# Performance work log

Hardware: AMD Instinct MI355X
Metric: run time of the kernel (lower is better)

The kernel has to match this reference:

```python
import jax, jax.numpy as jnp
from jax import lax
import numpy as np
import math

# --- static equivariant-conv basis (kernel lattice offsets) ---
K = 5          # kernel size = diameter / step
NRB = 3        # num_radial_basis
RMAX = 2.5     # diameter / 2
C0, C1 = 32, 16   # hidden irreps: 32x0e + 16x1e (4*ne scalars + 2*ne vectors, ne=8)
GATES = C1        # one 0e gate scalar per gated vector irrep

_c = np.arange(K, dtype=np.float32) - K // 2
_grid = np.stack(np.meshgrid(_c, _c, _c, indexing='ij'), -1)            # [K,K,K,3]
_norm = np.linalg.norm(_grid, axis=-1)
_mask = (_norm <= RMAX).astype(np.float32)
_ctr = np.linspace(0.0, RMAX, NRB).astype(np.float32)
_w = RMAX / (NRB - 1)
R_BASIS = jnp.asarray(np.exp(-(((_norm[..., None] - _ctr) / _w) ** 2)) * _mask[..., None])  # [K,K,K,NRB]
_safe = np.where(_norm == 0.0, 1.0, _norm)
_y1 = (math.sqrt(3.0) * _grid / _safe[..., None]).astype(np.float32)    # component-normalized l=1 SH
_y1[_norm == 0.0] = 0.0
Y1_SH = jnp.asarray(_y1)                                                # [K,K,K,3]
_levi = np.zeros((3, 3, 3), np.float32)
for _a, _b, _d in ((0, 1, 2), (1, 2, 0), (2, 0, 1)):
    _levi[_a, _b, _d] = 1.0
    _levi[_a, _d, _b] = -1.0
LEVI = jnp.asarray(_levi)


def _equiv_conv(x, ss, sv, vs, vv0, vv1):
    """Equivariant voxel conv: kernel = radial(|r|) * Y_l(r) * CG, then 3D conv.
    x: [B,D,H,W, C0 + 3*C1] -> [B,D,H,W, Cso + 3*Cvo]."""
    Cso, Cvo = ss.shape[-1], sv.shape[-1]
    Kss = jnp.einsum('xyzr,rio->xyzio', R_BASIS, ss)                      # 0e->0e via Y0
    Ksv = jnp.einsum('xyzr,rio,xyzm->xyziom', R_BASIS, sv, Y1_SH)         # 0e->1  via Y1
    Kvs = jnp.einsum('xyzr,rio,xyzm->xyzimo', R_BASIS, vs, Y1_SH) / math.sqrt(3.0)  # 1->0 (dot CG)
    Kvv0 = jnp.einsum('xyzr,rio->xyzio', R_BASIS, vv0)                    # 1->1 via Y0 (identity CG)
    Kvv1 = jnp.einsum('xyzr,rio->xyzio', R_BASIS, vv1)                    # 1->1 via Y1 (cross CG)
    E1 = jnp.einsum('xyzm,amb->xyzab', Y1_SH, LEVI) / math.sqrt(2.0)
    eye = jnp.eye(3, dtype=x.dtype)
    Kvv = (Kvv0[..., :, None, :, None] * eye[None, None, None, None, :, None, :]
           + Kvv1[..., :, None, :, None] * E1[..., None, :, None, :])     # [K,K,K,C1,3,Cvo,3]
    top = jnp.concatenate([Kss, Ksv.reshape(K, K, K, C0, 3 * Cvo)], axis=-1)
    bot = jnp.concatenate([Kvs.reshape(K, K, K, 3 * C1, Cso),
                           Kvv.reshape(K, K, K, 3 * C1, 3 * Cvo)], axis=-1)
    kern = jnp.concatenate([top, bot], axis=-2)                            # [K,K,K,Fin,Fout]
    return lax.conv_general_dilated(x, kern, (1, 1, 1), 'SAME',
                                    dimension_numbers=('NDHWC', 'DHWIO', 'NDHWC'))


def _gate(y):
    """e3nn Gate: activation on scalars, sigmoid(gates) scales the vectors."""
    s = jax.nn.relu(y[..., :C0])
    g = jax.nn.sigmoid(y[..., C0:C0 + GATES])
    v = y[..., C0 + GATES:].reshape(y.shape[:-1] + (C1, 3)) * g[..., None]
    return jnp.concatenate([s, v.reshape(y.shape[:-1] + (3 * C1,))], axis=-1)


def _up2(a, axes=(1, 2, 3)):
    for ax in axes:
        a = jnp.repeat(a, 2, axis=ax)
    return a


def _forward(x, c1_ss, c1_sv, c1_vs, c1_vv0, c1_vv1,
             c2_ss, c2_sv, c2_vs, c2_vv0, c2_vv1, w_pos, wl_s, wl_v):
    # --- ConvolutionBlock: two equivariant convs, each followed by a Gate ---
    x = _gate(_equiv_conv(x, c1_ss, c1_sv, c1_vs, c1_vv0, c1_vv1))
    x = _gate(_equiv_conv(x, c2_ss, c2_sv, c2_vs, c2_vv0, c2_vv1))
    B, Dc, Hc, Wc, _F = x.shape
    # --- _get_vectors: fine-grid offsets to (recentered) upsampled coarse centers ---
    ci = jnp.stack(jnp.meshgrid(jnp.arange(Dc), jnp.arange(Hc), jnp.arange(Wc), indexing='ij'), -1)
    centers = _up2((ci + jnp.array([Dc // 2, Hc // 2, Wc // 2]))[None], (1, 2, 3))[0].astype(jnp.float32)
    fi = jnp.stack(jnp.meshgrid(jnp.arange(2 * Dc), jnp.arange(2 * Hc), jnp.arange(2 * Wc),
                                indexing='ij'), -1).astype(jnp.float32)
    vecs = fi - centers                               # [2D,2H,2W,3]
    p = w_pos * vecs                                  # position_blocks: irreps-wise 1x1 Linear
    # --- nearest-neighbor upsample of features ---
    xu = _up2(x)                                      # [B,2D,2H,2W,F]
    S = xu[..., :C0]
    V = xu[..., C0:].reshape(xu.shape[:-1] + (C1, 3))
    # --- FullTensorProduct(features, pos embedding): per-voxel CG contractions ---
    t_s = jnp.einsum('bxyzcm,xyzm->bxyzc', V, p) / math.sqrt(3.0)          # 1x1->0
    t_v_sp = S[..., None] * p[None, :, :, :, None, :]                       # 0x1->1
    t_v_vp = jnp.cross(V, p[None, :, :, :, None, :]) / math.sqrt(2.0)       # 1x1->1
    tv = jnp.concatenate([t_v_sp, t_v_vp], axis=-2)                         # [...,C0+C1,3]
    # --- rebase_blocks_linear: irreps-wise Linear back to hidden (fan-in normalized) ---
    S_out = jnp.einsum('bxyzc,co->bxyzo', t_s, wl_s) / math.sqrt(C1)
    V_out = jnp.einsum('bxyzcm,co->bxyzom', tv, wl_v) / math.sqrt(C0 + C1)
    return jnp.concatenate([S_out, V_out.reshape(V_out.shape[:-2] + (3 * C1,))], axis=-1)


def setup_inputs() -> dict:
    key = jax.random.key(0)
    ks = jax.random.split(key, 16)
    n = jax.random.normal
    s = 0.02
    B, D = 1, 32
    FIN = C0 + 3 * C1          # 80
    CSO = C0 + GATES           # 48 output scalars (incl. gates) per conv
    return {
        'x': n(ks[0], (B, D, D, D, FIN), jnp.float32),
        'c1_ss': s * n(ks[1], (NRB, C0, CSO), jnp.float32),
        'c1_sv': s * n(ks[2], (NRB, C0, C1), jnp.float32),
        'c1_vs': s * n(ks[3], (NRB, C1, CSO), jnp.float32),
        'c1_vv0': s * n(ks[4], (NRB, C1, C1), jnp.float32),
        'c1_vv1': s * n(ks[5], (NRB, C1, C1), jnp.float32),
        'c2_ss': s * n(ks[6], (NRB, C0, CSO), jnp.float32),
        'c2_sv': s * n(ks[7], (NRB, C0, C1), jnp.float32),
        'c2_vs': s * n(ks[8], (NRB, C1, CSO), jnp.float32),
        'c2_vv0': s * n(ks[9], (NRB, C1, C1), jnp.float32),
        'c2_vv1': s * n(ks[10], (NRB, C1, C1), jnp.float32),
        'w_pos': 0.1 * n(ks[11], (), jnp.float32),
        'wl_s': n(ks[12], (C1, C0), jnp.float32),
        'wl_v': n(ks[13], (C0 + C1, C1), jnp.float32),
    }


def reference(x, c1_ss, c1_sv, c1_vs, c1_vv0, c1_vv1,
              c2_ss, c2_sv, c2_vs, c2_vv0, c2_vv1, w_pos, wl_s, wl_v):
    return _forward(x, c1_ss, c1_sv, c1_vs, c1_vv0, c1_vv1,
                    c2_ss, c2_sv, c2_vs, c2_vv0, c2_vv1, w_pos, wl_s, wl_v)
```

## Files before the change

kernel.cpp:

```cpp
#include <hip/hip_runtime.h>
#include <math.h>


typedef __attribute__((ext_vector_type(8))) short bf16x8;
typedef __attribute__((ext_vector_type(4))) float f32x4;

__device__ __forceinline__ int eps3(int a, int m, int b) {
    if (a == b || a == m || m == b) return 0;
    return ((a==0&&m==1&&b==2)||(a==1&&m==2&&b==0)||(a==2&&m==0&&b==1)) ? 1 : -1;
}

__global__ void build_tap(float* __restrict__ tap) {
    int t = threadIdx.x;
    if (t >= 125) return;
    int td = t / 25 - 2, th = (t / 5) % 5 - 2, tw = t % 5 - 2;
    int n2 = td*td + th*th + tw*tw;
    if (t == 62) {
        float* rec = tap + 40 * 16;
        rec[0] = __int_as_float(0); rec[1] = __int_as_float(0);
        for (int r = 0; r < 3; r++) {
            float tt = (0.f - 1.25f * (float)r) * 0.8f;
            rec[4 + r] = expf(-tt * tt);
        }
        return;
    }
    bool active = n2 <= 6;
    bool pos = (td > 0) || (td == 0 && th > 0) || (td == 0 && th == 0 && tw > 0);
    if (!(active && pos)) return;
    int idx = 0;
    for (int q = 0; q < t; q++) {
        int qd = q / 25 - 2, qh = (q / 5) % 5 - 2, qw = q % 5 - 2;
        int m2 = qd*qd + qh*qh + qw*qw;
        bool p = (qd > 0) || (qd == 0 && qh > 0) || (qd == 0 && qh == 0 && qw > 0);
        if (m2 <= 6 && p) idx++;
    }
    float* rec = tap + idx * 16;
    int off = td * 96 + th * 12 + tw;
    rec[0] = __int_as_float(off);
    rec[1] = __int_as_float(-off);
    float norm = sqrtf((float)n2);
    float comp[3] = {(float)td, (float)th, (float)tw};
    for (int r = 0; r < 3; r++) {
        float tt = (norm - 1.25f * (float)r) * 0.8f;
        float R = expf(-tt * tt);
        rec[4 + r] = R;
        for (int m = 0; m < 3; m++)
            rec[7 + r*3 + m] = R * 1.7320508075688772f * comp[m] / norm;
    }
}

__global__ void build_W(float* __restrict__ W,
    const float* __restrict__ ss1, const float* __restrict__ sv1,
    const float* __restrict__ vs1, const float* __restrict__ vv01, const float* __restrict__ vv11,
    const float* __restrict__ ss2, const float* __restrict__ sv2,
    const float* __restrict__ vs2, const float* __restrict__ vv02, const float* __restrict__ vv12)
{
    int idx = threadIdx.x + blockIdx.x * 256;
    if (idx >= 184320) return;
    int conv = idx / 92160;
    int rem  = idx % 92160;
    int j  = rem / 7680;
    int ci = (rem / 96) % 80;
    int co = rem % 96;
    int r = j >> 2, al = j & 3;
    const float* ss  = conv ? ss2  : ss1;
    const float* sv  = conv ? sv2  : sv1;
    const float* vs  = conv ? vs2  : vs1;
    const float* vv0 = conv ? vv02 : vv01;
    const float* vv1 = conv ? vv12 : vv11;
    float val = 0.f;
    if (ci < 32) {
        if (co < 48) { if (al == 0) val = ss[(r*32 + ci)*48 + co]; }
        else {
            int o = (co - 48) / 3, m = (co - 48) % 3;
            if (al == m + 1) val = sv[(r*32 + ci)*16 + o];
        }
    } else {
        int i = (ci - 32) / 3, a = (ci - 32) % 3;
        if (co < 48) { if (al == a + 1) val = vs[(r*16 + i)*48 + co] * 0.5773502691896258f; }
        else {
            int o = (co - 48) / 3, b = (co - 48) % 3;
            if (al == 0) { if (a == b) val = vv0[(r*16 + i)*16 + o]; }
            else {
                int e = eps3(a, al - 1, b);
                if (e) val = vv1[(r*16 + i)*16 + o] * (float)e * 0.7071067811865476f;
            }
        }
    }
    W[idx] = val;
}

__global__ void build_Wc(const float* __restrict__ W,
                         unsigned short* __restrict__ Wh, unsigned short* __restrict__ Wl)
{
    int idx = threadIdx.x + blockIdx.x * 256;
    if (idx >= 184320) return;
    int conv = idx / 92160, rem = idx % 92160;
    int co = rem / 960, kp = rem % 960;
    int c5 = kp / 192, r2 = kp % 192;
    int j = r2 / 16, ci16 = r2 % 16;
    int k = j * 80 + c5 * 16 + ci16;
    float w = W[conv * 92160 + k * 96 + co];
    unsigned int u = __float_as_uint(w);
    unsigned int hib = (u + 0x7FFFu + ((u >> 16) & 1u)) & 0xFFFF0000u;
    float res = w - __uint_as_float(hib);
    unsigned int v = __float_as_uint(res);
    unsigned int lob = (v + 0x7FFFu + ((v >> 16) & 1u)) >> 16;
    Wh[idx] = (unsigned short)(hib >> 16);
    Wl[idx] = (unsigned short)lob;
}

__device__ __forceinline__ void split8(float4 a, float4 b, bf16x8& hi, bf16x8& lo) {
    float av[8] = {a.x, a.y, a.z, a.w, b.x, b.y, b.z, b.w};
    #pragma unroll
    for (int e = 0; e < 8; e++) {
        unsigned int u = __float_as_uint(av[e]);
        hi[e] = (short)(u >> 16);
        float res = av[e] - __uint_as_float(u & 0xFFFF0000u);
        lo[e] = (short)(__float_as_uint(res) >> 16);
    }
}

__global__ __launch_bounds__(1024, 4) void fused_conv(
    const float* __restrict__ xin, const unsigned short* __restrict__ Wh,
    const unsigned short* __restrict__ Wl, const float* __restrict__ tap,
    float* __restrict__ xout)
{
    __shared__ float smem[37376];
    int tid = threadIdx.x;
    int vl = tid & 127, cg = tid >> 7;
    int dl = vl >> 5, hl = (vl >> 3) & 3, wl = vl & 7;
    int w16 = tid >> 6, l = tid & 63;
    int lr = l & 15, lk = l >> 4;
    int rt = w16 >> 1, nh = w16 & 1;
    int bid = blockIdx.x;
    int dt = (bid >> 5) << 2;
    int h0 = ((bid >> 2) & 7) << 2;
    int w0 = (bid & 3) << 3;

    int gof[3], lof[3];
    #pragma unroll
    for (int q = 0; q < 3; q++) {
        int i = tid + q * 1024;
        int sl = i / 768, rr = i - sl * 768;
        int dd = rr / 96, rm = rr - dd * 96;
        int hh = rm / 12, ww = rm - hh * 12;
        int gd = dt + dd - 2, gh = h0 + hh - 2, gw = w0 + ww - 2;
        gof[q] = (gd >= 0 && gd < 32 && gh >= 0 && gh < 32 && gw >= 0 && gw < 32)
               ? (((gd << 5) + gh) * 32 + gw) * 80 + sl * 4 : -1;
        lof[q] = sl * 3072 + rr * 4;
    }

    {
        float4 pf[3];
        #pragma unroll
        for (int q = 0; q < 3; q++)
            pf[q] = (gof[q] >= 0) ? *reinterpret_cast<const float4*>(xin + gof[q])
                                  : make_float4(0.f, 0.f, 0.f, 0.f);
        #pragma unroll
        for (int q = 0; q < 3; q++)
            *reinterpret_cast<float4*>(smem + lof[q]) = pf[q];
    }
    __syncthreads();

    const f32x4 fzero = {0.f, 0.f, 0.f, 0.f};
    f32x4 acc[3];
    #pragma unroll
    for (int nt = 0; nt < 3; nt++) acc[nt] = fzero;

    const float* xp = smem + (cg >> 1) * 3072
                    + (((dl + 2) * 8 + hl + 2) * 12 + (wl + 2)) * 4 + (cg & 1) * 2;
    float* zp = smem + 12288 + vl * 196 + cg * 2;
    const float* ap0 = smem + 12288 + (rt * 16 + lr) * 196 + lk * 8;

    for (int c5 = 0; c5 < 5; c5++) {
        float4 pf[3];
        if (c5 < 4) {
            int chof = (c5 + 1) * 16;
            #pragma unroll
            for (int q = 0; q < 3; q++)
                pf[q] = (gof[q] >= 0) ? *reinterpret_cast<const float4*>(xin + gof[q] + chof)
                                      : make_float4(0.f, 0.f, 0.f, 0.f);
        }
        {
            float az[12][2];
            #pragma unroll
            for (int j = 0; j < 12; j++) { az[j][0] = 0.f; az[j][1] = 0.f; }
            {
                const float* rec = tap + 640;
                float2 xc = *reinterpret_cast<const float2*>(xp);
                #pragma unroll
                for (int r = 0; r < 3; r++) {
                    float R = rec[4 + r];
                    az[r*4][0] += R * xc.x; az[r*4][1] += R * xc.y;
                }
            }
            for (int p = 0; p < 40; p++) {
                const float* rec = tap + p * 16;
                int op = __float_as_int(rec[0]) * 4, om = __float_as_int(rec[1]) * 4;
                float2 xa = *reinterpret_cast<const float2*>(xp + op);
                float2 xb = *reinterpret_cast<const float2*>(xp + om);
                float s0 = xa.x + xb.x, s1 = xa.y + xb.y;
                float d0 = xa.x - xb.x, d1 = xa.y - xb.y;
                #pragma unroll
                for (int r = 0; r < 3; r++) {
                    float R = rec[4 + r];
                    az[r*4][0] += R * s0; az[r*4][1] += R * s1;
                    #pragma unroll
                    for (int m = 0; m < 3; m++) {
                        float RY = rec[7 + r*3 + m];
                        az[r*4 + m + 1][0] += RY * d0;
                        az[r*4 + m + 1][1] += RY * d1;
                    }
                }
            }
            #pragma unroll
            for (int j = 0; j < 12; j++)
                *reinterpret_cast<float2*>(zp + j * 16) = make_float2(az[j][0], az[j][1]);
        }
        __syncthreads();
        if (c5 < 4) {
            #pragma unroll
            for (int q = 0; q < 3; q++)
                *reinterpret_cast<float4*>(smem + lof[q]) = pf[q];
        }
        #pragma unroll
        for (int ks = 0; ks < 6; ks++) {
            const unsigned short* bb = Wh + (nh * 48 + lr) * 960 + c5 * 192 + ks * 32 + lk * 8;
            const unsigned short* bbl = Wl + (nh * 48 + lr) * 960 + c5 * 192 + ks * 32 + lk * 8;
            bf16x8 bh[3], bl[3];
            #pragma unroll
            for (int nt = 0; nt < 3; nt++) {
                bh[nt] = *reinterpret_cast<const bf16x8*>(bb  + nt * 15360);
                bl[nt] = *reinterpret_cast<const bf16x8*>(bbl + nt * 15360);
            }
            const float* ap = ap0 + ks * 32;
            bf16x8 ah, al;
            split8(*reinterpret_cast<const float4*>(ap),
                   *reinterpret_cast<const float4*>(ap + 4), ah, al);
            #pragma unroll
            for (int nt = 0; nt < 3; nt++) {
                acc[nt] = __builtin_amdgcn_mfma_f32_16x16x32_bf16(ah, bh[nt], acc[nt], 0, 0, 0);
                acc[nt] = __builtin_amdgcn_mfma_f32_16x16x32_bf16(al, bh[nt], acc[nt], 0, 0, 0);
                acc[nt] = __builtin_amdgcn_mfma_f32_16x16x32_bf16(ah, bl[nt], acc[nt], 0, 0, 0);
            }
        }
        __syncthreads();
    }

    float* y = smem;
    #pragma unroll
    for (int nt = 0; nt < 3; nt++)
        #pragma unroll
        for (int r = 0; r < 4; r++)
            y[(rt * 16 + lk * 4 + r) * 98 + nh * 48 + nt * 16 + lr] = acc[nt][r];
    __syncthreads();
    #pragma unroll
    for (int it = 0; it < 10; it++) {
        int idx = tid + it * 1024;
        int vr = idx / 80, c = idx - vr * 80;
        int gd = dt + (vr >> 5), gh = h0 + ((vr >> 3) & 3), gw = w0 + (vr & 7);
        const float* yr = y + vr * 98;
        float val;
        if (c < 32) val = fmaxf(yr[c], 0.f);
        else {
            int q = c - 32;
            float g = 1.f / (1.f + __expf(-yr[32 + q / 3]));
            val = yr[48 + q] * g;
        }
        xout[(size_t)(((gd << 5) + gh) * 32 + gw) * 80 + c] = val;
    }
}

__global__ __launch_bounds__(256) void final_k(
    const float* __restrict__ x2, const float* __restrict__ wls,
    const float* __restrict__ wlv, const float* __restrict__ wpos,
    float* __restrict__ out)
{
    __shared__ float xv[16 * 81];
    __shared__ float coeff[16 * 161];
    __shared__ float s_wls[512];
    __shared__ float s_wlv[768];
    int t = threadIdx.x;
    int bid = blockIdx.x;
    int cw0 = (bid & 1) * 16;
    int ch  = (bid >> 1) & 31;
    int cd  = bid >> 6;
    float wp = wpos[0];
    {
        int base = ((cd * 32 + ch) * 32 + cw0) * 80;
        #pragma unroll
        for (int i = t; i < 1280; i += 256) {
            int vi = i / 80, c = i % 80;
            xv[vi * 81 + c] = x2[base + i];
        }
        for (int i = t; i < 512; i += 256) s_wls[i] = wls[i];
        for (int i = t; i < 768; i += 256) s_wlv[i] = wlv[i];
    }
    __syncthreads();
    {
        int vi = t >> 4, j = t & 15;
        const float* xp = xv + vi * 81;
        float* cf = coeff + vi * 161;
        #pragma unroll
        for (int l = 0; l < 10; l++) {
            int q = l * 16 + j;
            float sum = 0.f;
            if (q < 96) {
                int o = q / 3, m = q % 3;
                #pragma unroll
                for (int c = 0; c < 16; c++) sum += xp[32 + c * 3 + m] * s_wls[c * 32 + o];
            } else if (q < 112) {
                int o = q - 96;
                #pragma unroll
                for (int c = 0; c < 32; c++) sum += xp[c] * s_wlv[c * 16 + o];
            } else {
                int q2 = q - 112; int o = q2 / 3, m = q2 % 3;
                #pragma unroll
                for (int c = 0; c < 16; c++) sum += xp[32 + c * 3 + m] * s_wlv[(32 + c) * 16 + o];
            }
            cf[q] = sum;
        }
    }
    __syncthreads();
    const float scale = 0.14433756729740643f;
    #pragma unroll
    for (int f01 = 0; f01 < 4; f01++) {
        int fd = 2 * cd + (f01 >> 1), fh = 2 * ch + (f01 & 1);
        float p0 = wp * (float)(cd + (f01 >> 1) - 16);
        float p1 = wp * (float)(ch + (f01 & 1) - 16);
        size_t obase = (size_t)((fd * 64 + fh) * 64 + cw0 * 2) * 80;
        #pragma unroll
        for (int it = 0; it < 3; it++) {
            int idx4 = it * 256 + t;
            if (idx4 < 640) {
                int base = idx4 * 4;
                int fwl = base / 80, c0 = base - fwl * 80;
                int vi = fwl >> 1;
                float p2 = wp * (float)(cw0 + vi + (fwl & 1) - 16);
                const float* cf = coeff + vi * 161;
                float vv[4];
                if (c0 < 32) {
                    #pragma unroll
                    for (int e = 0; e < 4; e++) {
                        int c = c0 + e;
                        vv[e] = cf[c * 3] * p0 + cf[c * 3 + 1] * p1 + cf[c * 3 + 2] * p2;
                    }
                } else {
                    #pragma unroll
                    for (int e = 0; e < 4; e++) {
                        int q = c0 - 32 + e, o = q / 3, m = q - o * 3;
                        float A = cf[96 + o];
                        const float* w2 = cf + 112 + o * 3;
                        float pm, crm;
                        if (m == 0)      { pm = p0; crm = w2[1] * p2 - w2[2] * p1; }
                        else if (m == 1) { pm = p1; crm = w2[2] * p0 - w2[0] * p2; }
                        else             { pm = p2; crm = w2[0] * p1 - w2[1] * p0; }
                        vv[e] = A * pm + crm * 0.7071067811865476f;
                    }
                }
                *reinterpret_cast<float4*>(out + obase + base) =
                    make_float4(vv[0]*scale, vv[1]*scale, vv[2]*scale, vv[3]*scale);
            }
        }
    }
}

extern "C" void kernel_launch(void* const* d_in, const int* in_sizes, int n_in,
                              void* d_out, int out_size, void* d_ws, size_t ws_size,
                              hipStream_t stream)
{
    const float* x    = (const float*)d_in[0];
    const float* wpos = (const float*)d_in[11];
    const float* wls  = (const float*)d_in[12];
    const float* wlv  = (const float*)d_in[13];
    float* out = (float*)d_out;
    float* ws  = (float*)d_ws;

    float* tap = ws;
    float* W   = ws + 1024;
    unsigned short* Wh = (unsigned short*)(ws + 1024 + 184320);
    unsigned short* Wl = Wh + 184320;
    float* x1  = ws + 1024 + 184320 + 184320;
    float* x2  = x1 + 2621440;

    build_tap<<<1, 128, 0, stream>>>(tap);
    build_W<<<720, 256, 0, stream>>>(W,
        (const float*)d_in[1], (const float*)d_in[2], (const float*)d_in[3],
        (const float*)d_in[4], (const float*)d_in[5],
        (const float*)d_in[6], (const float*)d_in[7], (const float*)d_in[8],
        (const float*)d_in[9], (const float*)d_in[10]);
    build_Wc<<<720, 256, 0, stream>>>(W, Wh, Wl);

    fused_conv<<<256, 1024, 0, stream>>>(x,  Wh,         Wl,         tap, x1);
    fused_conv<<<256, 1024, 0, stream>>>(x1, Wh + 92160, Wl + 92160, tap, x2);
    final_k<<<2048, 256, 0, stream>>>(x2, wls, wlv, wpos, out);
}
```

Before: 411.3 us.

## Split block into two wave groups ping-ponging radial stencil and MFMA stages

Each workgroup is split into two halves of 8 waves. In every phase one half runs the VALU stencil (stage A) on its 64 voxels while the other half runs the MFMA GEMM (stage B) on the other 64 voxels' previous chunk, so vector ALU and matrix work can overlap. Stage A now splits each value into bf16 hi/lo once and stores them as packed bf16 in LDS using a swizzled layout. Stage B then reads them directly instead of re-splitting fp32. The input tile layout changes to a voxel-major stride of 18 floats to reduce bank conflicts, at the cost of extra barriers per chunk and a slightly larger LDS footprint.

```diff
diff --git a/kernel.cpp b/kernel.cpp
--- a/kernel.cpp
+++ b/kernel.cpp
@@ -35,7 +35,7 @@
         if (m2 <= 6 && p) idx++;
     }
     float* rec = tap + idx * 16;
-    int off = td * 96 + th * 12 + tw;
+    int off = (td * 96 + th * 12 + tw) * 18;
     rec[0] = __int_as_float(off);
     rec[1] = __int_as_float(-off);
     float norm = sqrtf((float)n2);
@@ -110,29 +110,117 @@
     Wl[idx] = (unsigned short)lob;
 }
 
-__device__ __forceinline__ void split8(float4 a, float4 b, bf16x8& hi, bf16x8& lo) {
-    float av[8] = {a.x, a.y, a.z, a.w, b.x, b.y, b.z, b.w};
-    #pragma unroll
-    for (int e = 0; e < 8; e++) {
-        unsigned int u = __float_as_uint(av[e]);
-        hi[e] = (short)(u >> 16);
-        float res = av[e] - __uint_as_float(u & 0xFFFF0000u);
-        lo[e] = (short)(__float_as_uint(res) >> 16);
-    }
-}
-
-__global__ __launch_bounds__(1024, 4) void fused_conv(
+
+__device__ __forceinline__ void stageA(
+    const float* __restrict__ smem, unsigned short* __restrict__ zch,
+    unsigned short* __restrict__ zcl, const float* __restrict__ tap,
+    int vox, int cg)
+{
+    int pos = ((vox >> 5) + 2) * 96 + ((((vox >> 3) & 3)) + 2) * 12 + (vox & 7) + 2;
+    const float* xp = smem + pos * 18 + 2 * cg;
+    float az[12][2];
+    #pragma unroll
+    for (int j = 0; j < 12; j++) { az[j][0] = 0.f; az[j][1] = 0.f; }
+    {
+        const float* rec = tap + 640;
+        float2 xc = *reinterpret_cast<const float2*>(xp);
+        #pragma unroll
+        for (int r = 0; r < 3; r++) {
+            float R = rec[4 + r];
+            az[r*4][0] += R * xc.x; az[r*4][1] += R * xc.y;
+        }
+    }
+    for (int p = 0; p < 40; p++) {
+        const float* rec = tap + p * 16;
+        int op = __float_as_int(rec[0]), om = __float_as_int(rec[1]);
+        float2 xa = *reinterpret_cast<const float2*>(xp + op);
+        float2 xb = *reinterpret_cast<const float2*>(xp + om);
+        float s0 = xa.x + xb.x, s1 = xa.y + xb.y;
+        float d0 = xa.x - xb.x, d1 = xa.y - xb.y;
+        #pragma unroll
+        for (int r = 0; r < 3; r++) {
+            float R = rec[4 + r];
+            az[r*4][0] += R * s0; az[r*4][1] += R * s1;
+            #pragma unroll
+            for (int m = 0; m < 3; m++) {
+                float RY = rec[7 + r*3 + m];
+                az[r*4 + m + 1][0] += RY * d0;
+                az[r*4 + m + 1][1] += RY * d1;
+            }
+        }
+    }
+    int swz = (vox >> 3) & 3;
+    int cg3 = cg & 3;
+    #pragma unroll
+    for (int j = 0; j < 12; j++) {
+        unsigned int hw = 0, lw = 0;
+        #pragma unroll
+        for (int e = 0; e < 2; e++) {
+            float a = az[j][e];
+            unsigned int u = __float_as_uint(a);
+            unsigned int hi = u >> 16;
+            float res = a - __uint_as_float(u & 0xFFFF0000u);
+            unsigned int lo2 = __float_as_uint(res) >> 16;
+            hw |= hi << (16 * e);
+            lw |= lo2 << (16 * e);
+        }
+        int k = j * 16 + 2 * cg;
+        int g = k >> 3;
+        int blk = g >> 2, sub = (g & 3) ^ swz;
+        int offu = vox * 200 + blk * 32 + sub * 8 + 2 * cg3;
+        *reinterpret_cast<unsigned int*>(zch + offu) = hw;
+        *reinterpret_cast<unsigned int*>(zcl + offu) = lw;
+    }
+}
+
+__device__ __forceinline__ void stageB(
+    const unsigned short* __restrict__ zch, const unsigned short* __restrict__ zcl,
+    const unsigned short* __restrict__ Wh, const unsigned short* __restrict__ Wl,
+    int c, int brow, int bnh, int lr, int lk, f32x4* acc)
+{
+    int swzB = (brow >> 3) & 3;
+    const unsigned short* zh = zch + brow * 200;
+    const unsigned short* zl = zcl + brow * 200;
+    const unsigned short* wb  = Wh + (bnh * 48 + lr) * 960 + c * 192 + lk * 8;
+    const unsigned short* wbl = Wl + (bnh * 48 + lr) * 960 + c * 192 + lk * 8;
+    int sub = (lk ^ swzB) * 8;
+    #pragma unroll
+    for (int ks = 0; ks < 6; ks++) {
+        bf16x8 bh[3], bl[3];
+        #pragma unroll
+        for (int nt = 0; nt < 3; nt++) {
+            bh[nt] = *reinterpret_cast<const bf16x8*>(wb  + nt * 15360 + ks * 32);
+            bl[nt] = *reinterpret_cast<const bf16x8*>(wbl + nt * 15360 + ks * 32);
+        }
+        int ao = ks * 32 + sub;
+        bf16x8 ah = *reinterpret_cast<const bf16x8*>(zh + ao);
+        bf16x8 al = *reinterpret_cast<const bf16x8*>(zl + ao);
+        #pragma unroll
+        for (int nt = 0; nt < 3; nt++) {
+            acc[nt] = __builtin_amdgcn_mfma_f32_16x16x32_bf16(ah, bh[nt], acc[nt], 0, 0, 0);
+            acc[nt] = __builtin_amdgcn_mfma_f32_16x16x32_bf16(al, bh[nt], acc[nt], 0, 0, 0);
+            acc[nt] = __builtin_amdgcn_mfma_f32_16x16x32_bf16(ah, bl[nt], acc[nt], 0, 0, 0);
+        }
+    }
+}
+
+__global__ __attribute__((amdgpu_flat_work_group_size(1024, 1024), amdgpu_waves_per_eu(4)))
+void fused_conv(
     const float* __restrict__ xin, const unsigned short* __restrict__ Wh,
     const unsigned short* __restrict__ Wl, const float* __restrict__ tap,
     float* __restrict__ xout)
 {
-    __shared__ float smem[37376];
+    __shared__ float smem[39424];
+    unsigned short* zch = reinterpret_cast<unsigned short*>(smem + 13824);
+    unsigned short* zcl = reinterpret_cast<unsigned short*>(smem + 26624);
     int tid = threadIdx.x;
-    int vl = tid & 127, cg = tid >> 7;
-    int dl = vl >> 5, hl = (vl >> 3) & 3, wl = vl & 7;
-    int w16 = tid >> 6, l = tid & 63;
+    int wv = tid >> 6, l = tid & 63;
     int lr = l & 15, lk = l >> 4;
-    int rt = w16 >> 1, nh = w16 & 1;
+    bool logrp = wv < 8;
+    int cg = wv & 7;
+    int brt = (wv & 7) >> 1, bnh = wv & 1;
+    int rowbase = (logrp ? 0 : 64) + brt * 16;
+    int brow = rowbase + lr;
     int bid = blockIdx.x;
     int dt = (bid >> 5) << 2;
     int h0 = ((bid >> 2) & 7) << 2;
@@ -148,7 +236,7 @@
         int gd = dt + dd - 2, gh = h0 + hh - 2, gw = w0 + ww - 2;
         gof[q] = (gd >= 0 && gd < 32 && gh >= 0 && gh < 32 && gw >= 0 && gw < 32)
                ? (((gd << 5) + gh) * 32 + gw) * 80 + sl * 4 : -1;
-        lof[q] = sl * 3072 + rr * 4;
+        lof[q] = rr * 18 + sl * 4;
     }
 
     {
@@ -158,8 +246,10 @@
             pf[q] = (gof[q] >= 0) ? *reinterpret_cast<const float4*>(xin + gof[q])
                                   : make_float4(0.f, 0.f, 0.f, 0.f);
         #pragma unroll
-        for (int q = 0; q < 3; q++)
-            *reinterpret_cast<float4*>(smem + lof[q]) = pf[q];
+        for (int q = 0; q < 3; q++) {
+            *reinterpret_cast<float2*>(smem + lof[q])     = make_float2(pf[q].x, pf[q].y);
+            *reinterpret_cast<float2*>(smem + lof[q] + 2) = make_float2(pf[q].z, pf[q].w);
+        }
     }
     __syncthreads();
 
@@ -168,92 +258,39 @@
     #pragma unroll
     for (int nt = 0; nt < 3; nt++) acc[nt] = fzero;
 
-    const float* xp = smem + (cg >> 1) * 3072
-                    + (((dl + 2) * 8 + hl + 2) * 12 + (wl + 2)) * 4 + (cg & 1) * 2;
-    float* zp = smem + 12288 + vl * 196 + cg * 2;
-    const float* ap0 = smem + 12288 + (rt * 16 + lr) * 196 + lk * 8;
-
-    for (int c5 = 0; c5 < 5; c5++) {
+    for (int c = 0; c < 5; c++) {
         float4 pf[3];
-        if (c5 < 4) {
-            int chof = (c5 + 1) * 16;
+        if (c < 4) {
+            int chof = (c + 1) * 16;
             #pragma unroll
             for (int q = 0; q < 3; q++)
                 pf[q] = (gof[q] >= 0) ? *reinterpret_cast<const float4*>(xin + gof[q] + chof)
                                       : make_float4(0.f, 0.f, 0.f, 0.f);
         }
-        {
-            float az[12][2];
+        if (logrp)      stageA(smem, zch, zcl, tap, l, cg);
+        else if (c > 0) stageB(zch, zcl, Wh, Wl, c - 1, brow, bnh, lr, lk, acc);
+        __syncthreads();
+        if (logrp) stageB(zch, zcl, Wh, Wl, c, brow, bnh, lr, lk, acc);
+        else       stageA(smem, zch, zcl, tap, 64 + l, cg);
+        __syncthreads();
+        if (c < 4) {
             #pragma unroll
-            for (int j = 0; j < 12; j++) { az[j][0] = 0.f; az[j][1] = 0.f; }
-            {
-                const float* rec = tap + 640;
-                float2 xc = *reinterpret_cast<const float2*>(xp);
-                #pragma unroll
-                for (int r = 0; r < 3; r++) {
-                    float R = rec[4 + r];
-                    az[r*4][0] += R * xc.x; az[r*4][1] += R * xc.y;
-                }
+            for (int q = 0; q < 3; q++) {
+                *reinterpret_cast<float2*>(smem + lof[q])     = make_float2(pf[q].x, pf[q].y);
+                *reinterpret_cast<float2*>(smem + lof[q] + 2) = make_float2(pf[q].z, pf[q].w);
             }
-            for (int p = 0; p < 40; p++) {
-                const float* rec = tap + p * 16;
-                int op = __float_as_int(rec[0]) * 4, om = __float_as_int(rec[1]) * 4;
-                float2 xa = *reinterpret_cast<const float2*>(xp + op);
-                float2 xb = *reinterpret_cast<const float2*>(xp + om);
-                float s0 = xa.x + xb.x, s1 = xa.y + xb.y;
-                float d0 = xa.x - xb.x, d1 = xa.y - xb.y;
-                #pragma unroll
-                for (int r = 0; r < 3; r++) {
-                    float R = rec[4 + r];
-                    az[r*4][0] += R * s0; az[r*4][1] += R * s1;
-                    #pragma unroll
-                    for (int m = 0; m < 3; m++) {
-                        float RY = rec[7 + r*3 + m];
-                        az[r*4 + m + 1][0] += RY * d0;
-                        az[r*4 + m + 1][1] += RY * d1;
-                    }
-                }
-            }
-            #pragma unroll
-            for (int j = 0; j < 12; j++)
-                *reinterpret_cast<float2*>(zp + j * 16) = make_float2(az[j][0], az[j][1]);
         }
         __syncthreads();
-        if (c5 < 4) {
-            #pragma unroll
-            for (int q = 0; q < 3; q++)
-                *reinterpret_cast<float4*>(smem + lof[q]) = pf[q];
-        }
-        #pragma unroll
-        for (int ks = 0; ks < 6; ks++) {
-            const unsigned short* bb = Wh + (nh * 48 + lr) * 960 + c5 * 192 + ks * 32 + lk * 8;
-            const unsigned short* bbl = Wl + (nh * 48 + lr) * 960 + c5 * 192 + ks * 32 + lk * 8;
-            bf16x8 bh[3], bl[3];
-            #pragma unroll
-            for (int nt = 0; nt < 3; nt++) {
-                bh[nt] = *reinterpret_cast<const bf16x8*>(bb  + nt * 15360);
-                bl[nt] = *reinterpret_cast<const bf16x8*>(bbl + nt * 15360);
-            }
-            const float* ap = ap0 + ks * 32;
-            bf16x8 ah, al;
-            split8(*reinterpret_cast<const float4*>(ap),
-                   *reinterpret_cast<const float4*>(ap + 4), ah, al);
-            #pragma unroll
-            for (int nt = 0; nt < 3; nt++) {
-                acc[nt] = __builtin_amdgcn_mfma_f32_16x16x32_bf16(ah, bh[nt], acc[nt], 0, 0, 0);
-                acc[nt] = __builtin_amdgcn_mfma_f32_16x16x32_bf16(al, bh[nt], acc[nt], 0, 0, 0);
-                acc[nt] = __builtin_amdgcn_mfma_f32_16x16x32_bf16(ah, bl[nt], acc[nt], 0, 0, 0);
-            }
-        }
-        __syncthreads();
-    }
+    }
+    if (!logrp) stageB(zch, zcl, Wh, Wl, 4, brow, bnh, lr, lk, acc);
+    __syncthreads();
 
     float* y = smem;
     #pragma unroll
     for (int nt = 0; nt < 3; nt++)
         #pragma unroll
         for (int r = 0; r < 4; r++)
-            y[(rt * 16 + lk * 4 + r) * 98 + nh * 48 + nt * 16 + lr] = acc[nt][r];
+            y[(rowbase + lk * 4 + r) * 98 + bnh * 48 + nt * 16 + lr] = acc[nt][r];
     __syncthreads();
     #pragma unroll
     for (int it = 0; it < 10; it++) {
```

New measurement: 371.0 us. 1.11x faster.
